# Kernel tuning notes

Measured on AMD Instinct MI355X. Metric: run time of the kernel, lower is better.

Reference implementation:

```python
import jax, jax.numpy as jnp
import numpy as np

B, S, D, H = 4, 2048, 1024, 16
HD = D // H

def setup_inputs() -> dict:
    key = jax.random.key(0)
    ks = jax.random.split(key, 11)
    s = 1.0 / np.sqrt(D)
    return {
        "q": jax.random.normal(ks[0], (B, S, D), jnp.float32),
        "k": jax.random.normal(ks[1], (B, S, D), jnp.float32),
        "v": jax.random.normal(ks[2], (B, S, D), jnp.float32),
        "Wq": jax.random.normal(ks[3], (D, D), jnp.float32) * s,
        "bq": jax.random.normal(ks[4], (D,), jnp.float32) * 0.01,
        "Wk": jax.random.normal(ks[5], (D, D), jnp.float32) * s,
        "bk": jax.random.normal(ks[6], (D,), jnp.float32) * 0.01,
        "Wv": jax.random.normal(ks[7], (D, D), jnp.float32) * s,
        "bv": jax.random.normal(ks[8], (D,), jnp.float32) * 0.01,
        "Wo": jax.random.normal(ks[9], (D, D), jnp.float32) * s,
        "bo": jax.random.normal(ks[10], (D,), jnp.float32) * 0.01,
    }

def reference(q, k, v, Wq, bq, Wk, bk, Wv, bv, Wo, bo):
    # linear projections + ReLU activation (as in the torch module)
    qh = jax.nn.relu(q @ Wq.T + bq)
    kh = jax.nn.relu(k @ Wk.T + bk)
    vh = jax.nn.relu(v @ Wv.T + bv)
    # split heads: [B,S,D] -> [B,H,S,HD]
    def split(x):
        return x.reshape(B, S, H, HD).transpose(0, 2, 1, 3)
    qh, kh, vh = split(qh), split(kh), split(vh)
    scale = 1.0 / np.sqrt(HD).astype(np.float32)
    scores = jnp.einsum("bhqd,bhkd->bhqk", qh, kh) * scale
    attn = jax.nn.softmax(scores, axis=-1)
    y = jnp.einsum("bhqk,bhkd->bhqd", attn, vh)
    # merge heads: [B,H,S,HD] -> [B,S,D]
    y = y.transpose(0, 2, 1, 3).reshape(B, S, D)
    return jax.nn.relu(y @ Wo.T + bo)
```

## Files before the change

### kernel.cpp

```cpp
#include <hip/hip_runtime.h>
#include <hip/hip_bf16.h>
#include <cstdint>
#include <cstddef>

#define Bc 4
#define Sc 2048
#define Dc 1024
#define Hc 16

typedef __bf16 bf16;
typedef bf16  bf16x4 __attribute__((ext_vector_type(4)));
typedef bf16  bf16x8 __attribute__((ext_vector_type(8)));
typedef float f32x4  __attribute__((ext_vector_type(4)));

__device__ __forceinline__ void load_lds16(const bf16* g, bf16* l) {
    __builtin_amdgcn_global_load_lds((const __attribute__((address_space(1))) void*)g,
                                     (__attribute__((address_space(3))) void*)l,
                                     16, 0, 0);
}

__device__ __forceinline__ void cvt16(const float* __restrict__ g,
                                      bf16x8& lo, bf16x8& hi) {
    const f32x4 a0 = *(const f32x4*)(g);
    const f32x4 a1 = *(const f32x4*)(g + 4);
    const f32x4 a2 = *(const f32x4*)(g + 8);
    const f32x4 a3 = *(const f32x4*)(g + 12);
#pragma unroll
    for (int j = 0; j < 4; j++) {
        lo[j]     = (bf16)a0[j];
        lo[j + 4] = (bf16)a1[j];
        hi[j]     = (bf16)a2[j];
        hi[j + 4] = (bf16)a3[j];
    }
}

__device__ __forceinline__ void store_relu(float* p, float v) { *p = fmaxf(v, 0.0f); }
__device__ __forceinline__ void store_relu(bf16*  p, float v) { *p = (bf16)fmaxf(v, 0.0f); }

__global__ __launch_bounds__(256)
void cvt_w4(const float* __restrict__ s0, const float* __restrict__ s1,
            const float* __restrict__ s2, const float* __restrict__ s3,
            bf16* __restrict__ dst) {
    const float* srcs[4] = {s0, s1, s2, s3};
    const float* src = srcs[blockIdx.y];
    const int idx = blockIdx.x * 256 + threadIdx.x;
    bf16x8 lo, hi;
    cvt16(src + (size_t)idx * 16, lo, hi);
    bf16* d = dst + (size_t)blockIdx.y * ((size_t)Dc * Dc) + (size_t)idx * 16;
    *(bf16x8*)d       = lo;
    *(bf16x8*)(d + 8) = hi;
}

#define BM 128
#define BN 64
#define BK 64

template <typename TC, bool TR, bool AF32>
__global__ __launch_bounds__(256)
void gemm_bb(const void* __restrict__ Av, const bf16* __restrict__ W,
             const float* __restrict__ bias, TC* __restrict__ C,
             int M, int N, int K) {
    __shared__ __align__(16) char pool[24576];
    bf16* lA = (bf16*)pool;
    bf16* lB = (bf16*)(pool + 16384);

    const int t    = threadIdx.x;
    const int lane = t & 63;
    const int wave = t >> 6;
    const int l15  = lane & 15;
    const int quad = lane >> 4;

    const int m0 = blockIdx.x * BM;
    const int n0 = blockIdx.y * BN;
    const int wm = (wave >> 1) * 64;
    const int wn = (wave & 1) * 32;

    f32x4 acc[4][2] = {};

    const int srow = t >> 3;
    const int cg   = (((t & 7) ^ (srow & 7)) << 3);
    const bf16*  gAb = (const bf16*)Av + (size_t)(m0 + srow) * K + cg;
    const float* gAf = (const float*)Av + (size_t)(m0 + srow) * K + cg;
    const bf16* gW = W + (size_t)(n0 + srow) * K + cg;
    bf16* lA0 = lA + t * 8;
    bf16* lB0 = lB + t * 8;

    f32x4 pre[8];
    if constexpr (AF32) {
#pragma unroll
        for (int c = 0; c < 4; c++) {
            const float* p = gAf + (size_t)(32 * c) * K;
            pre[2 * c]     = *(const f32x4*)p;
            pre[2 * c + 1] = *(const f32x4*)(p + 4);
        }
    }

    for (int k0 = 0; k0 < K; k0 += BK) {
        __syncthreads();
        if constexpr (AF32) {
#pragma unroll
            for (int c = 0; c < 4; c++) {
                bf16x8 w;
#pragma unroll
                for (int j = 0; j < 4; j++) {
                    w[j]     = (bf16)pre[2 * c][j];
                    w[j + 4] = (bf16)pre[2 * c + 1][j];
                }
                *(bf16x8*)(lA0 + c * 2048) = w;
            }
        } else {
#pragma unroll
            for (int c = 0; c < 4; c++)
                load_lds16(gAb + (size_t)(32 * c) * K + k0, lA0 + c * 2048);
        }
#pragma unroll
        for (int c = 0; c < 2; c++)
            load_lds16(gW + (size_t)(32 * c) * K, lB0 + c * 2048);
        gW += BK;
        __syncthreads();

        if constexpr (AF32) {
            if (k0 + BK < K) {
                const float* nA = gAf + (k0 + BK);
#pragma unroll
                for (int c = 0; c < 4; c++) {
                    const float* p = nA + (size_t)(32 * c) * K;
                    pre[2 * c]     = *(const f32x4*)p;
                    pre[2 * c + 1] = *(const f32x4*)(p + 4);
                }
            }
        }

#pragma unroll
        for (int ks = 0; ks < 2; ks++) {
            bf16x8 af[4], bfr[2];
            const int colp = ((((ks << 2) | quad) ^ (l15 & 7)) << 3);
#pragma unroll
            for (int mt = 0; mt < 4; mt++) {
                const int row = wm + mt * 16 + l15;
                af[mt] = *(const bf16x8*)(lA + row * BK + colp);
            }
#pragma unroll
            for (int nt = 0; nt < 2; nt++) {
                const int row = wn + nt * 16 + l15;
                bfr[nt] = *(const bf16x8*)(lB + row * BK + colp);
            }
#pragma unroll
            for (int mt = 0; mt < 4; mt++)
#pragma unroll
                for (int nt = 0; nt < 2; nt++)
                    acc[mt][nt] = __builtin_amdgcn_mfma_f32_16x16x32_bf16(
                        af[mt], bfr[nt], acc[mt][nt], 0, 0, 0);
        }
    }

    if constexpr (!TR) {
#pragma unroll
        for (int nt = 0; nt < 2; nt++) {
            const int col = n0 + wn + nt * 16 + l15;
            const float bv = bias[col];
#pragma unroll
            for (int mt = 0; mt < 4; mt++) {
                const int rowb = m0 + wm + mt * 16 + quad * 4;
#pragma unroll
                for (int i = 0; i < 4; i++)
                    store_relu(&C[(size_t)(rowb + i) * N + col], acc[mt][nt][i] + bv);
            }
        }
    } else {
        __syncthreads();
        bf16* trp = (bf16*)pool;
#pragma unroll
        for (int nt = 0; nt < 2; nt++) {
            const int col = n0 + wn + nt * 16 + l15;
            const float bv = bias[col];
#pragma unroll
            for (int mt = 0; mt < 4; mt++)
#pragma unroll
                for (int i = 0; i < 4; i++)
                    trp[((wave * 32) + nt * 16 + l15) * 72 + mt * 16 + quad * 4 + i] =
                        (bf16)fmaxf(acc[mt][nt][i] + bv, 0.0f);
        }
        __syncthreads();
        const int r2 = lane >> 3;
        const int c8 = (lane & 7) * 8;
#pragma unroll
        for (int rr = 0; rr < 4; rr++) {
            const int rt = rr * 8 + r2;
            const bf16x8 vv = *(const bf16x8*)&trp[((wave * 32) + rt) * 72 + c8];
            const int cg2 = n0 + wn + rt;
            const int h   = cg2 >> 6, hd = cg2 & 63;
            const int mg  = m0 + wm + c8;
            const int b   = mg >> 11, s = mg & (Sc - 1);
            bf16* dst = (bf16*)C + ((size_t)(b * Hc + h) * 64 + hd) * Sc + s;
            *(bf16x8*)dst = vv;
        }
    }
}

#define QI 4

__global__ __launch_bounds__(256)
void attn_flash(const bf16* __restrict__ Qh, const bf16* __restrict__ Kh,
                const bf16* __restrict__ Vt_g, bf16* __restrict__ Y) {
    __shared__ __align__(16) bf16 Kl[64][72];
    __shared__ __align__(16) bf16 Vl[64][72];
    __shared__ __align__(16) bf16 Pl[4][64][72];

    const int t    = threadIdx.x;
    const int lane = t & 63;
    const int wave = t >> 6;
    const int l15  = lane & 15;
    const int quad = lane >> 4;

    const int bh = blockIdx.x;
    const int qt = blockIdx.y;
    const int b  = bh >> 4;
    const int h  = bh & 15;
    const int q0 = qt * 256;
    const size_t rowbase = (size_t)b * Sc;
    const size_t vhead   = (size_t)(b * Hc + h) * 64;

    const float qscale = 0.125f * 1.44269504f;
    bf16x8 qf[QI][2];
#pragma unroll
    for (int qi = 0; qi < QI; qi++) {
        const bf16* qp = Qh + (rowbase + q0 + wave * 64 + qi * 16 + l15) * (size_t)Dc + h * 64;
#pragma unroll
        for (int ks = 0; ks < 2; ks++) {
            const bf16x8 raw = *(const bf16x8*)(qp + ks * 32 + quad * 8);
#pragma unroll
            for (int j = 0; j < 8; j++) qf[qi][ks][j] = (bf16)((float)raw[j] * qscale);
        }
    }

    bf16x8 ones;
#pragma unroll
    for (int j = 0; j < 8; j++) ones[j] = (bf16)1.0f;

    f32x4 yacc[QI][4] = {};
    f32x4 sacc[QI]    = {};

    const int sr = t >> 2;
    const int sc = (t & 3) * 16;
    constexpr int NT = Sc / 64;

    const bf16* kp = Kh + (rowbase + sr) * (size_t)Dc + h * 64 + sc;
    const bf16* vp = Vt_g + (vhead + sr) * (size_t)Sc + sc;
    bf16x8 k0 = *(const bf16x8*)kp;
    bf16x8 k1 = *(const bf16x8*)(kp + 8);
    bf16x8 v0 = *(const bf16x8*)vp;
    bf16x8 v1 = *(const bf16x8*)(vp + 8);

    for (int kt = 0; kt < NT; kt++) {
        __syncthreads();
        *(bf16x8*)&Kl[sr][sc]     = k0;
        *(bf16x8*)&Kl[sr][sc + 8] = k1;
        *(bf16x8*)&Vl[sr][sc]     = v0;
        *(bf16x8*)&Vl[sr][sc + 8] = v1;
        __syncthreads();

        if (kt + 1 < NT) {
            kp += (size_t)64 * Dc;
            vp += 64;
            k0 = *(const bf16x8*)kp;
            k1 = *(const bf16x8*)(kp + 8);
            v0 = *(const bf16x8*)vp;
            v1 = *(const bf16x8*)(vp + 8);
        }

        bf16x8 kf[4][2];
#pragma unroll
        for (int mt = 0; mt < 4; mt++) {
            kf[mt][0] = *(const bf16x8*)&Kl[mt * 16 + l15][quad * 8];
            kf[mt][1] = *(const bf16x8*)&Kl[mt * 16 + l15][32 + quad * 8];
        }

#pragma unroll
        for (int qi = 0; qi < QI; qi++) {
            f32x4 s[4];
            __builtin_amdgcn_s_setprio(1);
#pragma unroll
            for (int mt = 0; mt < 4; mt++) {
                s[mt] = (f32x4){0.f, 0.f, 0.f, 0.f};
                s[mt] = __builtin_amdgcn_mfma_f32_16x16x32_bf16(
                    kf[mt][0], qf[qi][0], s[mt], 0, 0, 0);
                s[mt] = __builtin_amdgcn_mfma_f32_16x16x32_bf16(
                    kf[mt][1], qf[qi][1], s[mt], 0, 0, 0);
            }
            __builtin_amdgcn_s_setprio(0);
#pragma unroll
            for (int mt = 0; mt < 4; mt++) {
                bf16x4 pk;
#pragma unroll
                for (int i = 0; i < 4; i++)
                    pk[i] = (bf16)__builtin_amdgcn_exp2f(s[mt][i]);
                *(bf16x4*)&Pl[wave][qi * 16 + l15][mt * 16 + quad * 4] = pk;
            }
        }

        bf16x8 vf[4][2];
#pragma unroll
        for (int nt = 0; nt < 4; nt++) {
            vf[nt][0] = *(const bf16x8*)&Vl[nt * 16 + l15][quad * 8];
            vf[nt][1] = *(const bf16x8*)&Vl[nt * 16 + l15][32 + quad * 8];
        }

        bf16x8 pf[QI][2];
#pragma unroll
        for (int qi = 0; qi < QI; qi++) {
            pf[qi][0] = *(const bf16x8*)&Pl[wave][qi * 16 + l15][quad * 8];
            pf[qi][1] = *(const bf16x8*)&Pl[wave][qi * 16 + l15][32 + quad * 8];
        }
        __builtin_amdgcn_s_setprio(1);
#pragma unroll
        for (int qi = 0; qi < QI; qi++) {
            sacc[qi] = __builtin_amdgcn_mfma_f32_16x16x32_bf16(ones, pf[qi][0], sacc[qi], 0, 0, 0);
            sacc[qi] = __builtin_amdgcn_mfma_f32_16x16x32_bf16(ones, pf[qi][1], sacc[qi], 0, 0, 0);
#pragma unroll
            for (int nt = 0; nt < 4; nt++) {
                yacc[qi][nt] = __builtin_amdgcn_mfma_f32_16x16x32_bf16(
                    vf[nt][0], pf[qi][0], yacc[qi][nt], 0, 0, 0);
                yacc[qi][nt] = __builtin_amdgcn_mfma_f32_16x16x32_bf16(
                    vf[nt][1], pf[qi][1], yacc[qi][nt], 0, 0, 0);
            }
        }
        __builtin_amdgcn_s_setprio(0);
    }

#pragma unroll
    for (int qi = 0; qi < QI; qi++) {
        const float inv = 1.0f / sacc[qi][0];
        bf16* yp = Y + (rowbase + q0 + wave * 64 + qi * 16 + l15) * (size_t)Dc + h * 64;
#pragma unroll
        for (int nt = 0; nt < 4; nt++)
#pragma unroll
            for (int i = 0; i < 4; i++)
                yp[nt * 16 + quad * 4 + i] = (bf16)(yacc[qi][nt][i] * inv);
    }
}

extern "C" void kernel_launch(void* const* d_in, const int* in_sizes, int n_in,
                              void* d_out, int out_size, void* d_ws, size_t ws_size,
                              hipStream_t stream) {
    const float* q  = (const float*)d_in[0];
    const float* k  = (const float*)d_in[1];
    const float* v  = (const float*)d_in[2];
    const float* Wq = (const float*)d_in[3];
    const float* bq = (const float*)d_in[4];
    const float* Wk = (const float*)d_in[5];
    const float* bk = (const float*)d_in[6];
    const float* Wv = (const float*)d_in[7];
    const float* bv = (const float*)d_in[8];
    const float* Wo = (const float*)d_in[9];
    const float* bo = (const float*)d_in[10];
    float* out = (float*)d_out;

    const int M = Bc * Sc;
    const int N = Dc;
    const int K = Dc;
    const size_t E  = (size_t)Bc * Sc * Dc;
    const size_t EW = (size_t)Dc * Dc;

    bf16* Qh   = (bf16*)d_out;
    bf16* Kh   = Qh + E;
    bf16* tmpA = (bf16*)d_ws;
    bf16* VtG  = tmpA + E;
    bf16* Wqb  = VtG + E;
    bf16* Wkb  = Wqb + EW;
    bf16* Wvb  = Wkb + EW;
    bf16* Wob  = Wvb + EW;

    const int n16w = (int)(EW / 16);
    dim3 gw4(n16w / 256, 4);
    dim3 gg(M / BM, N / BN);
    dim3 ga(Bc * Hc, Sc / 256);

    cvt_w4<<<gw4, 256, 0, stream>>>(Wq, Wk, Wv, Wo, Wqb);

    gemm_bb<bf16, false, true><<<gg, 256, 0, stream>>>(q, Wqb, bq, Qh, M, N, K);
    gemm_bb<bf16, false, true><<<gg, 256, 0, stream>>>(k, Wkb, bk, Kh, M, N, K);
    gemm_bb<bf16, true,  true><<<gg, 256, 0, stream>>>(v, Wvb, bv, VtG, M, N, K);

    attn_flash<<<ga, 256, 0, stream>>>(Qh, Kh, VtG, tmpA);

    gemm_bb<float, false, false><<<gg, 256, 0, stream>>>(tmpA, Wob, bo, out, M, N, K);
}
```

Measured before the change: 382.7 us.

## Double-buffer LDS in GEMMs and batch QKV projections into one launch

New measurement: 385.3 us. About the same (+0.7%).

```diff
diff --git a/kernel.cpp b/kernel.cpp
--- a/kernel.cpp
+++ b/kernel.cpp
@@ -54,21 +54,28 @@
 #define BM 128
 #define BN 64
 #define BK 64
-
-template <typename TC, bool TR, bool AF32>
+#define KITERS 16
+
 __global__ __launch_bounds__(256)
-void gemm_bb(const void* __restrict__ Av, const bf16* __restrict__ W,
-             const float* __restrict__ bias, TC* __restrict__ C,
-             int M, int N, int K) {
-    __shared__ __align__(16) char pool[24576];
+void gemm_qkv(const float* __restrict__ Aq, const float* __restrict__ Ak,
+              const float* __restrict__ Avv, const bf16* __restrict__ Wall,
+              const float* __restrict__ bq, const float* __restrict__ bk,
+              const float* __restrict__ bv, bf16* __restrict__ Cqk,
+              bf16* __restrict__ vtg, int M, int N, int K) {
+    __shared__ __align__(16) char pool[49152];
     bf16* lA = (bf16*)pool;
-    bf16* lB = (bf16*)(pool + 16384);
+    bf16* lB = (bf16*)(pool + 32768);
 
     const int t    = threadIdx.x;
     const int lane = t & 63;
     const int wave = t >> 6;
     const int l15  = lane & 15;
     const int quad = lane >> 4;
+    const int z    = blockIdx.z;
+
+    const float* A = (z == 0) ? Aq : (z == 1) ? Ak : Avv;
+    const bf16*  W = Wall + (size_t)z * ((size_t)Dc * Dc);
+    const float* bias = (z == 0) ? bq : (z == 1) ? bk : bv;
 
     const int m0 = blockIdx.x * BM;
     const int n0 = blockIdx.y * BN;
@@ -79,25 +86,40 @@
 
     const int srow = t >> 3;
     const int cg   = (((t & 7) ^ (srow & 7)) << 3);
-    const bf16*  gAb = (const bf16*)Av + (size_t)(m0 + srow) * K + cg;
-    const float* gAf = (const float*)Av + (size_t)(m0 + srow) * K + cg;
-    const bf16* gW = W + (size_t)(n0 + srow) * K + cg;
-    bf16* lA0 = lA + t * 8;
-    bf16* lB0 = lB + t * 8;
+    const float* gAf = A + (size_t)(m0 + srow) * K + cg;
+    const bf16*  gW  = W + (size_t)(n0 + srow) * K + cg;
 
     f32x4 pre[8];
-    if constexpr (AF32) {
-#pragma unroll
-        for (int c = 0; c < 4; c++) {
-            const float* p = gAf + (size_t)(32 * c) * K;
-            pre[2 * c]     = *(const f32x4*)p;
-            pre[2 * c + 1] = *(const f32x4*)(p + 4);
-        }
-    }
-
-    for (int k0 = 0; k0 < K; k0 += BK) {
-        __syncthreads();
-        if constexpr (AF32) {
+#pragma unroll
+    for (int c = 0; c < 4; c++) {
+        const float* p = gAf + (size_t)(32 * c) * K;
+        pre[2 * c]     = *(const f32x4*)p;
+        pre[2 * c + 1] = *(const f32x4*)(p + 4);
+    }
+#pragma unroll
+    for (int c = 0; c < 4; c++) {
+        bf16x8 w;
+#pragma unroll
+        for (int j = 0; j < 4; j++) {
+            w[j]     = (bf16)pre[2 * c][j];
+            w[j + 4] = (bf16)pre[2 * c + 1][j];
+        }
+        *(bf16x8*)(lA + t * 8 + c * 2048) = w;
+    }
+#pragma unroll
+    for (int c = 0; c < 2; c++)
+        load_lds16(gW + (size_t)(32 * c) * K, lB + t * 8 + c * 2048);
+#pragma unroll
+    for (int c = 0; c < 4; c++) {
+        const float* p = gAf + (size_t)(32 * c) * K + BK;
+        pre[2 * c]     = *(const f32x4*)p;
+        pre[2 * c + 1] = *(const f32x4*)(p + 4);
+    }
+    __syncthreads();
+
+    for (int tI = 0; tI < KITERS; tI++) {
+        const int cu = tI & 1, nx = cu ^ 1;
+        if (tI + 1 < KITERS) {
 #pragma unroll
             for (int c = 0; c < 4; c++) {
                 bf16x8 w;
@@ -106,31 +128,21 @@
                     w[j]     = (bf16)pre[2 * c][j];
                     w[j + 4] = (bf16)pre[2 * c + 1][j];
                 }
-                *(bf16x8*)(lA0 + c * 2048) = w;
-            }
-        } else {
-#pragma unroll
-            for (int c = 0; c < 4; c++)
-                load_lds16(gAb + (size_t)(32 * c) * K + k0, lA0 + c * 2048);
-        }
-#pragma unroll
-        for (int c = 0; c < 2; c++)
-            load_lds16(gW + (size_t)(32 * c) * K, lB0 + c * 2048);
-        gW += BK;
-        __syncthreads();
-
-        if constexpr (AF32) {
-            if (k0 + BK < K) {
-                const float* nA = gAf + (k0 + BK);
+                *(bf16x8*)(lA + nx * 8192 + t * 8 + c * 2048) = w;
+            }
+#pragma unroll
+            for (int c = 0; c < 2; c++)
+                load_lds16(gW + (size_t)(32 * c) * K + (tI + 1) * BK,
+                           lB + nx * 4096 + t * 8 + c * 2048);
+            if (tI + 2 < KITERS) {
 #pragma unroll
                 for (int c = 0; c < 4; c++) {
-                    const float* p = nA + (size_t)(32 * c) * K;
+                    const float* p = gAf + (size_t)(32 * c) * K + (tI + 2) * BK;
                     pre[2 * c]     = *(const f32x4*)p;
                     pre[2 * c + 1] = *(const f32x4*)(p + 4);
                 }
             }
         }
-
 #pragma unroll
         for (int ks = 0; ks < 2; ks++) {
             bf16x8 af[4], bfr[2];
@@ -138,12 +150,12 @@
 #pragma unroll
             for (int mt = 0; mt < 4; mt++) {
                 const int row = wm + mt * 16 + l15;
-                af[mt] = *(const bf16x8*)(lA + row * BK + colp);
+                af[mt] = *(const bf16x8*)(lA + cu * 8192 + row * BK + colp);
             }
 #pragma unroll
             for (int nt = 0; nt < 2; nt++) {
                 const int row = wn + nt * 16 + l15;
-                bfr[nt] = *(const bf16x8*)(lB + row * BK + colp);
+                bfr[nt] = *(const bf16x8*)(lB + cu * 4096 + row * BK + colp);
             }
 #pragma unroll
             for (int mt = 0; mt < 4; mt++)
@@ -152,19 +164,21 @@
                     acc[mt][nt] = __builtin_amdgcn_mfma_f32_16x16x32_bf16(
                         af[mt], bfr[nt], acc[mt][nt], 0, 0, 0);
         }
-    }
-
-    if constexpr (!TR) {
+        __syncthreads();
+    }
+
+    if (z < 2) {
+        bf16* C = Cqk + (size_t)z * ((size_t)Bc * Sc * Dc);
 #pragma unroll
         for (int nt = 0; nt < 2; nt++) {
             const int col = n0 + wn + nt * 16 + l15;
-            const float bv = bias[col];
+            const float bvv = bias[col];
 #pragma unroll
             for (int mt = 0; mt < 4; mt++) {
                 const int rowb = m0 + wm + mt * 16 + quad * 4;
 #pragma unroll
                 for (int i = 0; i < 4; i++)
-                    store_relu(&C[(size_t)(rowb + i) * N + col], acc[mt][nt][i] + bv);
+                    store_relu(&C[(size_t)(rowb + i) * N + col], acc[mt][nt][i] + bvv);
             }
         }
     } else {
@@ -173,13 +187,13 @@
 #pragma unroll
         for (int nt = 0; nt < 2; nt++) {
             const int col = n0 + wn + nt * 16 + l15;
-            const float bv = bias[col];
+            const float bvv = bias[col];
 #pragma unroll
             for (int mt = 0; mt < 4; mt++)
 #pragma unroll
                 for (int i = 0; i < 4; i++)
                     trp[((wave * 32) + nt * 16 + l15) * 72 + mt * 16 + quad * 4 + i] =
-                        (bf16)fmaxf(acc[mt][nt][i] + bv, 0.0f);
+                        (bf16)fmaxf(acc[mt][nt][i] + bvv, 0.0f);
         }
         __syncthreads();
         const int r2 = lane >> 3;
@@ -192,8 +206,92 @@
             const int h   = cg2 >> 6, hd = cg2 & 63;
             const int mg  = m0 + wm + c8;
             const int b   = mg >> 11, s = mg & (Sc - 1);
-            bf16* dst = (bf16*)C + ((size_t)(b * Hc + h) * 64 + hd) * Sc + s;
+            bf16* dst = vtg + ((size_t)(b * Hc + h) * 64 + hd) * Sc + s;
             *(bf16x8*)dst = vv;
+        }
+    }
+}
+
+__global__ __launch_bounds__(256)
+void gemm_out(const bf16* __restrict__ A, const bf16* __restrict__ W,
+              const float* __restrict__ bias, float* __restrict__ C,
+              int M, int N, int K) {
+    __shared__ __align__(16) char pool[49152];
+    bf16* lA = (bf16*)pool;
+    bf16* lB = (bf16*)(pool + 32768);
+
+    const int t    = threadIdx.x;
+    const int lane = t & 63;
+    const int wave = t >> 6;
+    const int l15  = lane & 15;
+    const int quad = lane >> 4;
+
+    const int m0 = blockIdx.x * BM;
+    const int n0 = blockIdx.y * BN;
+    const int wm = (wave >> 1) * 64;
+    const int wn = (wave & 1) * 32;
+
+    f32x4 acc[4][2] = {};
+
+    const int srow = t >> 3;
+    const int cg   = (((t & 7) ^ (srow & 7)) << 3);
+    const bf16* gA = A + (size_t)(m0 + srow) * K + cg;
+    const bf16* gW = W + (size_t)(n0 + srow) * K + cg;
+
+#pragma unroll
+    for (int c = 0; c < 4; c++)
+        load_lds16(gA + (size_t)(32 * c) * K, lA + t * 8 + c * 2048);
+#pragma unroll
+    for (int c = 0; c < 2; c++)
+        load_lds16(gW + (size_t)(32 * c) * K, lB + t * 8 + c * 2048);
+    __syncthreads();
+
+    for (int tI = 0; tI < KITERS; tI++) {
+        const int cu = tI & 1, nx = cu ^ 1;
+        if (tI + 1 < KITERS) {
+#pragma unroll
+            for (int c = 0; c < 4; c++)
+                load_lds16(gA + (size_t)(32 * c) * K + (tI + 1) * BK,
+                           lA + nx * 8192 + t * 8 + c * 2048);
+#pragma unroll
+            for (int c = 0; c < 2; c++)
+                load_lds16(gW + (size_t)(32 * c) * K + (tI + 1) * BK,
+                           lB + nx * 4096 + t * 8 + c * 2048);
+        }
+#pragma unroll
+        for (int ks = 0; ks < 2; ks++) {
+            bf16x8 af[4], bfr[2];
+            const int colp = ((((ks << 2) | quad) ^ (l15 & 7)) << 3);
+#pragma unroll
+            for (int mt = 0; mt < 4; mt++) {
+                const int row = wm + mt * 16 + l15;
+                af[mt] = *(const bf16x8*)(lA + cu * 8192 + row * BK + colp);
+            }
+#pragma unroll
+            for (int nt = 0; nt < 2; nt++) {
+                const int row = wn + nt * 16 + l15;
+                bfr[nt] = *(const bf16x8*)(lB + cu * 4096 + row * BK + colp);
+            }
+#pragma unroll
+            for (int mt = 0; mt < 4; mt++)
+#pragma unroll
+                for (int nt = 0; nt < 2; nt++)
+                    acc[mt][nt] = __builtin_amdgcn_mfma_f32_16x16x32_bf16(
+                        af[mt], bfr[nt], acc[mt][nt], 0, 0, 0);
+        }
+        __syncthreads();
+    }
+
+#pragma unroll
+    for (int nt = 0; nt < 2; nt++) {
+        const int col = n0 + wn + nt * 16 + l15;
+        const float bvv = bias[col];
+#pragma unroll
+        for (int mt = 0; mt < 4; mt++) {
+            const int rowb = m0 + wm + mt * 16 + quad * 4;
+#pragma unroll
+            for (int i = 0; i < 4; i++)
+                store_relu(&C[(size_t)(rowb + i) * N + col], acc[mt][nt][i] + bvv);
         }
     }
 }
@@ -363,26 +461,22 @@
     const size_t EW = (size_t)Dc * Dc;
 
     bf16* Qh   = (bf16*)d_out;
-    bf16* Kh   = Qh + E;
     bf16* tmpA = (bf16*)d_ws;
     bf16* VtG  = tmpA + E;
     bf16* Wqb  = VtG + E;
-    bf16* Wkb  = Wqb + EW;
-    bf16* Wvb  = Wkb + EW;
-    bf16* Wob  = Wvb + EW;
+    bf16* Wob  = Wqb + 3 * EW;
 
     const int n16w = (int)(EW / 16);
     dim3 gw4(n16w / 256, 4);
-    dim3 gg(M / BM, N / BN);
+    dim3 gg3(M / BM, N / BN, 3);
+    dim3 ggo(M / BM, N / BN);
     dim3 ga(Bc * Hc, Sc / 256);
 
     cvt_w4<<<gw4, 256, 0, stream>>>(Wq, Wk, Wv, Wo, Wqb);
 
-    gemm_bb<bf16, false, true><<<gg, 256, 0, stream>>>(q, Wqb, bq, Qh, M, N, K);
-    gemm_bb<bf16, false, true><<<gg, 256, 0, stream>>>(k, Wkb, bk, Kh, M, N, K);
-    gemm_bb<bf16, true,  true><<<gg, 256, 0, stream>>>(v, Wvb, bv, VtG, M, N, K);
-
-    attn_flash<<<ga, 256, 0, stream>>>(Qh, Kh, VtG, tmpA);
-
-    gemm_bb<float, false, false><<<gg, 256, 0, stream>>>(tmpA, Wob, bo, out, M, N, K);
-}
+    gemm_qkv<<<gg3, 256, 0, stream>>>(q, k, v, Wqb, bq, bk, bv, Qh, VtG, M, N, K);
+
+    attn_flash<<<ga, 256, 0, stream>>>(Qh, Qh + E, VtG, tmpA);
+
+    gemm_out<<<ggo, 256, 0, stream>>>(tmpA, Wob, bo, out, M, N, K);
+}
```
